# Optimization experiments

Measured on AMD Instinct MI355X. Metric: run time of the kernel, lower is better.

The kernel has to match this reference:

```python
import jax, jax.numpy as jnp
import numpy as np

B = 1024      # batch
DF = 2048     # dim_feat (hard-coded in module)
DIM = 128     # contrastive feature dim
C = 8192      # class_num
P = 8         # pos_size_per_cls
N = 4         # neg_size_per_cls
BN_EPS = 1e-5


def _l2norm(x, axis):
    n = jnp.sqrt(jnp.sum(x * x, axis=axis, keepdims=True))
    return x / jnp.maximum(n, 1e-12)


def setup_inputs() -> dict:
    key = jax.random.key(0)
    ks = jax.random.split(key, 12)
    inp = {
        'mid_feat_q': jax.random.normal(ks[0], (B, DF), jnp.float32),
        'mid_feat_k': jax.random.normal(ks[1], (B, DF), jnp.float32),
        'labels_q': jax.random.randint(ks[2], (B,), 0, C, jnp.int32),
        'labels_k': jax.random.randint(ks[3], (B,), 0, C, jnp.int32),
        'W1': jax.random.normal(ks[4], (DF, DF), jnp.float32) * 0.02,
        'b1': jnp.zeros((DF,), jnp.float32),
        'gamma': jnp.ones((DF,), jnp.float32),
        'beta': jnp.zeros((DF,), jnp.float32),
        'W2': jax.random.normal(ks[5], (DF, DIM), jnp.float32) * 0.02,
        'b2': jnp.zeros((DIM,), jnp.float32),
        'Wlin': jax.random.normal(ks[6], (DF, C), jnp.float32) * 0.02,
        'blin': jnp.zeros((C,), jnp.float32),
        'neg_queue': _l2norm(jax.random.normal(ks[7], (DIM, N * C), jnp.float32), axis=0),
        'pos_queue': _l2norm(jax.random.normal(ks[8], (DIM, P * C), jnp.float32), axis=0),
        'neg_ptr': jnp.zeros((C,), jnp.int32),
        'pos_ptr': jnp.zeros((C,), jnp.int32),
    }
    return inp


def _mlp(x, W1, b1, gamma, beta, W2, b2):
    # Linear -> BatchNorm1d (training: batch stats, biased var) -> ReLU -> Linear
    h = x @ W1 + b1
    mu = jnp.mean(h, axis=0)
    var = jnp.var(h, axis=0)
    h = (h - mu) * jax.lax.rsqrt(var + BN_EPS) * gamma + beta
    h = jax.nn.relu(h)
    return h @ W2 + b2


def reference(mid_feat_q, mid_feat_k, labels_q, labels_k,
              W1, b1, gamma, beta, W2, b2, Wlin, blin,
              neg_queue, pos_queue, neg_ptr, pos_ptr):
    feat_q = _l2norm(_mlp(mid_feat_q, W1, b1, gamma, beta, W2, b2), axis=1)
    feat_k = _l2norm(_mlp(mid_feat_k, W1, b1, gamma, beta, W2, b2), axis=1)

    # per-sample positive block gather: pos_queue[:, l*P:(l+1)*P]
    posq = pos_queue.reshape(DIM, C, P)          # (dim, C, P)
    pg = posq[:, labels_q, :]                    # (dim, B, P)
    pos_list = jnp.einsum('bd,dbp->bp', feat_q, pg)   # (B, P)

    # negatives: full sim then drop each sample's own-class block of N columns
    full_neg = feat_q @ neg_queue                # (B, N*C)
    cols = jnp.arange(N * (C - 1), dtype=jnp.int32)
    idx = cols[None, :] + N * (cols[None, :] >= labels_q[:, None] * N).astype(jnp.int32)
    neg_list = jnp.take_along_axis(full_neg, idx, axis=1)  # (B, N*(C-1))

    sim_batch = feat_q @ feat_k.T                # (B, B)
    labels_batch = (labels_q[:, None] == labels_k[None, :]).astype(jnp.float32)

    sim_con = jnp.concatenate([sim_batch, pos_list, neg_list], axis=1)
    labels_con = jnp.concatenate(
        [labels_batch, jnp.ones_like(pos_list), jnp.zeros_like(neg_list)], axis=1)

    logit_cls_q = mid_feat_q @ Wlin + blin
    logit_cls_k = mid_feat_k @ Wlin + blin

    # sequential dequeue/enqueue over the key batch (world_size=1 all_gather)
    def step(carry, inp):
        nq, nptr, pq, pptr = carry
        kv, c = inp
        npos = nptr[c]
        nq = nq.at[:, c * N + npos].set(kv)
        nptr = nptr.at[c].set((npos + 1) % N)
        ppos = pptr[c]
        pq = pq.at[:, c * P + ppos].set(kv)
        pptr = pptr.at[c].set((ppos + 1) % P)
        return (nq, nptr, pq, pptr), None

    (neg_queue2, neg_ptr2, pos_queue2, pos_ptr2), _ = jax.lax.scan(
        step, (neg_queue, neg_ptr, pos_queue, pos_ptr),
        (jax.lax.stop_gradient(feat_k), labels_k))

    return (sim_con, labels_con, logit_cls_q, logit_cls_k,
            neg_queue2, pos_queue2, neg_ptr2, pos_ptr2)
```

## Files before the change

kernel.cpp:

```cpp
#include <hip/hip_runtime.h>

typedef unsigned short u16;
typedef __bf16 bf16x8 __attribute__((ext_vector_type(8)));
typedef unsigned short ushort8 __attribute__((ext_vector_type(8)));
typedef float f32x4 __attribute__((ext_vector_type(4)));

typedef const __attribute__((address_space(1))) void gv_t;
typedef __attribute__((address_space(3))) void lv_t;

__device__ __forceinline__ u16 f2bf(float f) {
    union { float f; unsigned u; } x; x.f = f;
    unsigned r = x.u + 0x7fffu + ((x.u >> 16) & 1u);
    return (u16)(r >> 16);
}
__device__ __forceinline__ float bf2f(u16 h) {
    union { unsigned u; float f; } x; x.u = ((unsigned)h) << 16; return x.f;
}
__device__ __forceinline__ bf16x8 as_bf(ushort8 u) {
    union { ushort8 u; bf16x8 b; } x; x.u = u; return x.b;
}

__global__ void k_cast2(const float* __restrict__ in0, const float* __restrict__ in1,
                        u16* __restrict__ out0, u16* __restrict__ out1, long nvec) {
    const float* in = blockIdx.y ? in1 : in0;
    u16* out = blockIdx.y ? out1 : out0;
    long i = (long)blockIdx.x * blockDim.x + threadIdx.x;
    long stride = (long)gridDim.x * blockDim.x;
    for (; i < nvec; i += stride) {
        float4 v = ((const float4*)in)[i];
        u16 o[4] = {f2bf(v.x), f2bf(v.y), f2bf(v.z), f2bf(v.w)};
        *(unsigned long long*)(out + i * 4) = *(unsigned long long*)o;
    }
}

__global__ void k_castT(const float* __restrict__ in, u16* __restrict__ out,
                        int R, int C) {
    __shared__ u16 tile[32][33];
    int c0 = blockIdx.x * 32, r0 = blockIdx.y * 32;
    int tx = threadIdx.x, ty = threadIdx.y;
#pragma unroll
    for (int i = 0; i < 4; i++)
        tile[ty + 8 * i][tx] = f2bf(in[(size_t)(r0 + ty + 8 * i) * C + c0 + tx]);
    __syncthreads();
#pragma unroll
    for (int i = 0; i < 4; i++)
        out[(size_t)(c0 + ty + 8 * i) * R + r0 + tx] = tile[tx][ty + 8 * i];
}

template <int EPI>
__global__ __launch_bounds__(256, 2) void gemm_bt(
    const u16* A0, const u16* A1, const u16* __restrict__ Bt,
    const float* __restrict__ bias, u16* H0, u16* H1, float* C0, float* C1,
    int lda, int ldb, long long ldc, int n_tiles, int Kchunk,
    const int* __restrict__ labels) {
    __shared__ u16 Al[128 * 32];
    __shared__ u16 Bl[128 * 32];
    const int bx = blockIdx.x;
    const int by = blockIdx.y % n_tiles;
    const int kc = blockIdx.y / n_tiles;
    const int half = blockIdx.z;
    const u16* A = half ? A1 : A0;
    const int m0 = bx * 128, n0 = by * 128;
    const int t = threadIdx.x;
    const int w = t >> 6, l = t & 63;
    const int wm = (w & 1) * 64, wn = (w >> 1) * 64;
    const int quad = l >> 4, ln = l & 15;
    const int srow = t >> 2;
    const int sk = (t & 3) * 8;

    f32x4 acc[4][4];
#pragma unroll
    for (int i = 0; i < 4; i++)
#pragma unroll
        for (int j = 0; j < 4; j++) acc[i][j] = f32x4{};

    u16* lAw = Al + (w << 4) * 32;
    u16* lBw = Bl + (w << 4) * 32;

    const int k_begin = kc * Kchunk;
    for (int k0 = k_begin; k0 < k_begin + Kchunk; k0 += 32) {
        if (k0 != k_begin) __syncthreads();
#pragma unroll
        for (int i = 0; i < 2; i++) {
            __builtin_amdgcn_global_load_lds(
                (gv_t*)(A + (size_t)(m0 + srow + i * 64) * lda + k0 + sk),
                (lv_t*)(lAw + i * 64 * 32), 16, 0, 0);
            __builtin_amdgcn_global_load_lds(
                (gv_t*)(Bt + (size_t)(n0 + srow + i * 64) * ldb + k0 + sk),
                (lv_t*)(lBw + i * 64 * 32), 16, 0, 0);
        }
        __syncthreads();
        bf16x8 af[4], bb[4];
#pragma unroll
        for (int i = 0; i < 4; i++) {
            af[i] = as_bf(*(const ushort8*)(Al + (wm + i * 16 + ln) * 32 + quad * 8));
            bb[i] = as_bf(*(const ushort8*)(Bl + (wn + i * 16 + ln) * 32 + quad * 8));
        }
#pragma unroll
        for (int i = 0; i < 4; i++)
#pragma unroll
            for (int j = 0; j < 4; j++)
                acc[i][j] = __builtin_amdgcn_mfma_f32_16x16x32_bf16(af[i], bb[j], acc[i][j], 0, 0, 0);
    }

    u16* Hs = half ? H1 : H0;
    float* Cs = half ? C1 : C0;
#pragma unroll
    for (int i = 0; i < 4; i++) {
        int row = m0 + wm + i * 16 + quad * 4;
#pragma unroll
        for (int j = 0; j < 4; j++) {
            int col = n0 + wn + j * 16 + ln;
            float bv = 0.f;
            if (EPI == 0 || EPI == 3) { if (bias) bv = bias[col]; }
#pragma unroll
            for (int r = 0; r < 4; r++) {
                int rr = row + r;
                float v = acc[i][j][r] + bv;
                if (EPI == 0) {
                    Cs[(size_t)rr * ldc + col] = v;
                } else if (EPI == 3) {
                    Hs[(size_t)rr * ldc + col] = f2bf(v);
                } else if (EPI == 2) {
                    Cs[(size_t)kc * (1024 * (size_t)ldc) + (size_t)rr * ldc + col] = v;
                } else {
                    int L4 = labels[rr] * 4;
                    if (col < L4)
                        Cs[(size_t)rr * ldc + 1032 + col] = v;
                    else if (col >= L4 + 4)
                        Cs[(size_t)rr * ldc + 1032 + col - 4] = v;
                }
            }
        }
    }
}

__global__ void k_bn_stats(const u16* __restrict__ Hq, const u16* __restrict__ Hk,
                           float* __restrict__ ps, float* __restrict__ ps2) {
    int half = blockIdx.z;
    const u16* H = half ? Hk : Hq;
    int col = blockIdx.x * 256 + threadIdx.x;
    int r0 = blockIdx.y * 64;
    float s = 0.f, s2 = 0.f;
    for (int r = 0; r < 64; r++) {
        float v = bf2f(H[(size_t)(r0 + r) * 2048 + col]);
        s += v; s2 += v * v;
    }
    size_t o = ((size_t)half * 16 + blockIdx.y) * 2048 + col;
    ps[o] = s; ps2[o] = s2;
}

__global__ void k_bn_final(const float* __restrict__ ps, const float* __restrict__ ps2,
                           const float* __restrict__ gamma, const float* __restrict__ beta,
                           float* __restrict__ scale, float* __restrict__ shift) {
    int idx = blockIdx.x * 256 + threadIdx.x;
    int half = idx >> 11, col = idx & 2047;
    float s = 0.f, s2 = 0.f;
    for (int rb = 0; rb < 16; rb++) {
        size_t o = ((size_t)half * 16 + rb) * 2048 + col;
        s += ps[o]; s2 += ps2[o];
    }
    float mu = s * (1.f / 1024.f);
    float var = s2 * (1.f / 1024.f) - mu * mu;
    float sc = gamma[col] * rsqrtf(var + 1e-5f);
    shift[half * 2048 + col] = beta[col] - mu * sc;
    scale[half * 2048 + col] = sc;
}

__global__ void k_bn_apply(u16* Hq, u16* Hk, const float* __restrict__ scale,
                           const float* __restrict__ shift) {
    int row = blockIdx.x, half = blockIdx.y;
    u16* H = half ? Hk : Hq;
    int col = threadIdx.x * 8;
    ushort8 h = *(ushort8*)(H + (size_t)row * 2048 + col);
    ushort8 o;
#pragma unroll
    for (int k = 0; k < 8; k++) {
        float v = bf2f(h[k]) * scale[half * 2048 + col + k] + shift[half * 2048 + col + k];
        o[k] = f2bf(fmaxf(v, 0.f));
    }
    *(ushort8*)(H + (size_t)row * 2048 + col) = o;
}

__global__ void k_l2norm(const float* __restrict__ Fqp, const float* __restrict__ Fkp,
                         const float* __restrict__ b2, float* fqf, float* fkf,
                         u16* fqh, u16* fkh, const float* __restrict__ pq,
                         const int* __restrict__ lq, float* __restrict__ out0) {
    int row = blockIdx.x, half = blockIdx.y, d = threadIdx.x;
    const float* Fp = half ? Fkp : Fqp;
    float x = b2[d];
#pragma unroll
    for (int kc = 0; kc < 8; kc++)
        x += Fp[(size_t)kc * 131072 + (size_t)row * 128 + d];
    float ss = x * x;
#pragma unroll
    for (int off = 32; off >= 1; off >>= 1) ss += __shfl_down(ss, off);
    __shared__ float p[2];
    if ((threadIdx.x & 63) == 0) p[threadIdx.x >> 6] = ss;
    __syncthreads();
    float n = sqrtf(p[0] + p[1]);
    float v = x / fmaxf(n, 1e-12f);
    (half ? fkf : fqf)[(size_t)row * 128 + d] = v;
    (half ? fkh : fqh)[(size_t)row * 128 + d] = f2bf(v);

    if (half == 0) {
        int base = lq[row] * 8;
        const float* pp = pq + (size_t)d * 65536 + base;
        float4 v0 = *(const float4*)pp;
        float4 v1 = *(const float4*)(pp + 4);
        float a[8] = {v * v0.x, v * v0.y, v * v0.z, v * v0.w,
                      v * v1.x, v * v1.y, v * v1.z, v * v1.w};
#pragma unroll
        for (int off = 32; off >= 1; off >>= 1)
#pragma unroll
            for (int q = 0; q < 8; q++) a[q] += __shfl_down(a[q], off);
        __shared__ float pr[2][8];
        if ((threadIdx.x & 63) == 0) {
#pragma unroll
            for (int q = 0; q < 8; q++) pr[threadIdx.x >> 6][q] = a[q];
        }
        __syncthreads();
        if (threadIdx.x < 8)
            out0[(size_t)row * 33796 + 1024 + threadIdx.x] =
                pr[0][threadIdx.x] + pr[1][threadIdx.x];
    }
}

__global__ void k_labels(const int* __restrict__ lq, const int* __restrict__ lk,
                         float* __restrict__ out1) {
    int b = blockIdx.y;
    int j0 = (blockIdx.x * 256 + threadIdx.x) * 8;
    if (j0 >= 33796) return;
    float* o = out1 + (size_t)b * 33796;
    if (j0 >= 1032 && j0 + 8 <= 33796) {
        float4 z = {0.f, 0.f, 0.f, 0.f};
        *(float4*)(o + j0) = z;
        *(float4*)(o + j0 + 4) = z;
    } else {
        int Lq = lq[b];
        for (int k = 0; k < 8 && j0 + k < 33796; k++) {
            int j = j0 + k;
            o[j] = (j < 1024) ? ((Lq == lk[j]) ? 1.f : 0.f) : (j < 1032 ? 1.f : 0.f);
        }
    }
}

__global__ void k_copy2(const float* __restrict__ s1, float* __restrict__ d1, long n1,
                        const float* __restrict__ s2, float* __restrict__ d2, long n2) {
    long i = (long)blockIdx.x * blockDim.x + threadIdx.x;
    long stride = (long)gridDim.x * blockDim.x;
    long tot = n1 + n2;
    for (; i < tot; i += stride) {
        if (i < n1) ((float4*)d1)[i] = ((const float4*)s1)[i];
        else ((float4*)d2)[i - n1] = ((const float4*)s2)[i - n1];
    }
}

__global__ void k_rank(const int* __restrict__ lk, const int* __restrict__ nptr,
                       const int* __restrict__ pptr, int* __restrict__ counts,
                       int* __restrict__ colN, int* __restrict__ colP) {
    __shared__ int lab[1024];
    int tid = threadIdx.x;
    for (int i = tid; i < 1024; i += 128) lab[i] = lk[i];
    __syncthreads();
    int b = blockIdx.x * 128 + tid;
    int c = lab[b];
    int rank = 0, count = 0;
    for (int i = 0; i < 1024; i++) {
        int m = (lab[i] == c);
        count += m;
        rank += (i < b) ? m : 0;
    }
    if (rank == count - 1) counts[c] = count;
    colN[b] = (rank >= count - 4) ? c * 4 + (nptr[c] + rank) % 4 : -1;
    colP[b] = (rank >= count - 8) ? c * 8 + (pptr[c] + rank) % 8 : -1;
}

__global__ void k_scatter(const float* __restrict__ fkf, const int* __restrict__ colN,
                          const int* __restrict__ colP, float* outN, float* outP) {
    int b = blockIdx.x, d = threadIdx.x;
    float v = fkf[(size_t)b * 128 + d];
    int cn = colN[b];
    if (cn >= 0) outN[(size_t)d * 32768 + cn] = v;
    int cp = colP[b];
    if (cp >= 0) outP[(size_t)d * 65536 + cp] = v;
}

__global__ void k_ptrs(const int* __restrict__ nptr, const int* __restrict__ pptr,
                       const int* __restrict__ counts, float* outN, float* outP) {
    int c = blockIdx.x * 256 + threadIdx.x;
    int cnt = counts[c];
    outN[c] = (float)((nptr[c] + cnt) & 3);
    outP[c] = (float)((pptr[c] + cnt) & 7);
}

extern "C" void kernel_launch(void* const* d_in, const int* in_sizes, int n_in,
                              void* d_out, int out_size, void* d_ws, size_t ws_size,
                              hipStream_t stream) {
    const float* midq = (const float*)d_in[0];
    const float* midk = (const float*)d_in[1];
    const int* lq     = (const int*)d_in[2];
    const int* lk     = (const int*)d_in[3];
    const float* W1   = (const float*)d_in[4];
    const float* b1   = (const float*)d_in[5];
    const float* gamma= (const float*)d_in[6];
    const float* beta = (const float*)d_in[7];
    const float* W2   = (const float*)d_in[8];
    const float* b2   = (const float*)d_in[9];
    const float* Wlin = (const float*)d_in[10];
    const float* blin = (const float*)d_in[11];
    const float* nq   = (const float*)d_in[12];
    const float* pq   = (const float*)d_in[13];
    const int* nptr   = (const int*)d_in[14];
    const int* pptr   = (const int*)d_in[15];
    (void)in_sizes; (void)n_in; (void)out_size; (void)ws_size;

    float* out = (float*)d_out;
    const size_t O0 = 0;
    const size_t O1 = 34607104;
    const size_t O2 = 69214208;
    const size_t O3 = 77602816;
    const size_t O4 = 85991424;
    const size_t O5 = 90185728;
    const size_t O6 = 98574336;
    const size_t O7 = 98582528;

    char* ws = (char*)d_ws;
    size_t off = 0;
    auto alloc = [&](size_t bytes) -> char* {
        char* p = ws + off;
        off = (off + bytes + 255) & ~(size_t)255;
        return p;
    };
    u16* W1t   = (u16*)alloc((size_t)2048 * 2048 * 2);
    u16* WlinT = (u16*)alloc((size_t)8192 * 2048 * 2);
    u16* W2t   = (u16*)alloc((size_t)128 * 2048 * 2);
    u16* nqT   = (u16*)alloc((size_t)32768 * 128 * 2);
    u16* midqh = (u16*)alloc((size_t)1024 * 2048 * 2);
    u16* midkh = (u16*)alloc((size_t)1024 * 2048 * 2);
    u16* Hq    = (u16*)alloc((size_t)1024 * 2048 * 2);
    u16* Hk    = (u16*)alloc((size_t)1024 * 2048 * 2);
    float* Fq  = (float*)alloc((size_t)8 * 1024 * 128 * 4);
    float* Fk  = (float*)alloc((size_t)8 * 1024 * 128 * 4);
    float* fqf = (float*)alloc((size_t)1024 * 128 * 4);
    float* fkf = (float*)alloc((size_t)1024 * 128 * 4);
    u16* fqh   = (u16*)alloc((size_t)1024 * 128 * 2);
    u16* fkh   = (u16*)alloc((size_t)1024 * 128 * 2);
    float* ps  = (float*)alloc((size_t)2 * 16 * 2048 * 4);
    float* ps2 = (float*)alloc((size_t)2 * 16 * 2048 * 4);
    float* scaleA = (float*)alloc((size_t)2 * 2048 * 4);
    float* shiftA = (float*)alloc((size_t)2 * 2048 * 4);
    int* counts = (int*)alloc(8192 * 4);
    int* colN   = (int*)alloc(1024 * 4);
    int* colP   = (int*)alloc(1024 * 4);

    k_cast2<<<dim3(1024, 2), 256, 0, stream>>>(midq, midk, midqh, midkh,
                                               (long)1024 * 2048 / 4);
    dim3 tb(32, 8);
    k_castT<<<dim3(64, 64), tb, 0, stream>>>(W1, W1t, 2048, 2048);
    k_castT<<<dim3(256, 64), tb, 0, stream>>>(Wlin, WlinT, 2048, 8192);
    k_castT<<<dim3(4, 64), tb, 0, stream>>>(W2, W2t, 2048, 128);
    k_castT<<<dim3(1024, 4), tb, 0, stream>>>(nq, nqT, 128, 32768);

    gemm_bt<3><<<dim3(8, 16, 2), 256, 0, stream>>>(midqh, midkh, W1t, b1, Hq, Hk,
        nullptr, nullptr, 2048, 2048, 2048, 16, 2048, nullptr);

    k_bn_stats<<<dim3(8, 16, 2), 256, 0, stream>>>(Hq, Hk, ps, ps2);
    k_bn_final<<<16, 256, 0, stream>>>(ps, ps2, gamma, beta, scaleA, shiftA);
    k_bn_apply<<<dim3(1024, 2), 256, 0, stream>>>(Hq, Hk, scaleA, shiftA);

    hipMemsetAsync(counts, 0, 8192 * 4, stream);

    gemm_bt<2><<<dim3(8, 8, 2), 256, 0, stream>>>(Hq, Hk, W2t, nullptr, nullptr,
        nullptr, Fq, Fk, 2048, 2048, 128, 1, 256, nullptr);

    k_l2norm<<<dim3(1024, 2), 128, 0, stream>>>(Fq, Fk, b2, fqf, fkf, fqh, fkh,
                                                pq, lq, out + O0);

    gemm_bt<0><<<dim3(8, 8, 1), 256, 0, stream>>>(fqh, fqh, fkh, nullptr,
        nullptr, nullptr, out + O0, out + O0, 128, 128, 33796, 8, 128, nullptr);

    gemm_bt<1><<<dim3(8, 256, 1), 256, 0, stream>>>(fqh, fqh, nqT, nullptr,
        nullptr, nullptr, out + O0, out + O0, 128, 128, 33796, 256, 128, lq);

    k_labels<<<dim3(17, 1024), 256, 0, stream>>>(lq, lk, out + O1);

    gemm_bt<0><<<dim3(8, 64, 2), 256, 0, stream>>>(midqh, midkh, WlinT, blin,
        nullptr, nullptr, out + O2, out + O3, 2048, 2048, 8192, 64, 2048, nullptr);

    k_copy2<<<2048, 256, 0, stream>>>(nq, out + O4, 4194304 / 4,
                                      pq, out + O5, 8388608 / 4);

    k_rank<<<8, 128, 0, stream>>>(lk, nptr, pptr, counts, colN, colP);
    k_scatter<<<1024, 128, 0, stream>>>(fkf, colN, colP, out + O4, out + O5);
    k_ptrs<<<32, 256, 0, stream>>>(nptr, pptr, counts, out + O6, out + O7);
}
```

Baseline: 775.9 us.

## Double GEMM K-tile to 64 with XOR-swizzled LDS; fuse BN-stats and scatter kernels

The bf16 MFMA GEMM now stages 64-wide K slices per iteration instead of 32. Rows are written into LDS with an XOR swizzle of 8-element chunks, and fragments are read back with the matching swizzle. This halves the barrier and load-issue overhead per unit of K and is meant to cut LDS bank conflicts on fragment reads. BatchNorm statistics are computed in one kernel, with each thread summing all 1024 rows of a column, which drops the partial-sum buffers and a launch but runs only 16 blocks. The queue scatter and pointer-update kernels are merged into one launch.

```diff
diff --git a/kernel.cpp b/kernel.cpp
--- a/kernel.cpp
+++ b/kernel.cpp
@@ -53,8 +53,8 @@
     const float* __restrict__ bias, u16* H0, u16* H1, float* C0, float* C1,
     int lda, int ldb, long long ldc, int n_tiles, int Kchunk,
     const int* __restrict__ labels) {
-    __shared__ u16 Al[128 * 32];
-    __shared__ u16 Bl[128 * 32];
+    __shared__ u16 Al[128 * 64];
+    __shared__ u16 Bl[128 * 64];
     const int bx = blockIdx.x;
     const int by = blockIdx.y % n_tiles;
     const int kc = blockIdx.y / n_tiles;
@@ -65,8 +65,8 @@
     const int w = t >> 6, l = t & 63;
     const int wm = (w & 1) * 64, wn = (w >> 1) * 64;
     const int quad = l >> 4, ln = l & 15;
-    const int srow = t >> 2;
-    const int sk = (t & 3) * 8;
+    const int srow = t >> 3;
+    const int spos = t & 7;
 
     f32x4 acc[4][4];
 #pragma unroll
@@ -74,33 +74,38 @@
 #pragma unroll
         for (int j = 0; j < 4; j++) acc[i][j] = f32x4{};
 
-    u16* lAw = Al + (w << 4) * 32;
-    u16* lBw = Bl + (w << 4) * 32;
+    const int swz = ln & 7;
 
     const int k_begin = kc * Kchunk;
-    for (int k0 = k_begin; k0 < k_begin + Kchunk; k0 += 32) {
+    for (int k0 = k_begin; k0 < k_begin + Kchunk; k0 += 64) {
         if (k0 != k_begin) __syncthreads();
 #pragma unroll
-        for (int i = 0; i < 2; i++) {
+        for (int i = 0; i < 4; i++) {
+            int r = i * 32 + srow;
+            int c = (spos ^ (r & 7)) * 8;
             __builtin_amdgcn_global_load_lds(
-                (gv_t*)(A + (size_t)(m0 + srow + i * 64) * lda + k0 + sk),
-                (lv_t*)(lAw + i * 64 * 32), 16, 0, 0);
+                (gv_t*)(A + (size_t)(m0 + r) * lda + k0 + c),
+                (lv_t*)(Al + i * 2048 + t * 8), 16, 0, 0);
             __builtin_amdgcn_global_load_lds(
-                (gv_t*)(Bt + (size_t)(n0 + srow + i * 64) * ldb + k0 + sk),
-                (lv_t*)(lBw + i * 64 * 32), 16, 0, 0);
+                (gv_t*)(Bt + (size_t)(n0 + r) * ldb + k0 + c),
+                (lv_t*)(Bl + i * 2048 + t * 8), 16, 0, 0);
         }
         __syncthreads();
-        bf16x8 af[4], bb[4];
-#pragma unroll
-        for (int i = 0; i < 4; i++) {
-            af[i] = as_bf(*(const ushort8*)(Al + (wm + i * 16 + ln) * 32 + quad * 8));
-            bb[i] = as_bf(*(const ushort8*)(Bl + (wn + i * 16 + ln) * 32 + quad * 8));
-        }
-#pragma unroll
-        for (int i = 0; i < 4; i++)
-#pragma unroll
-            for (int j = 0; j < 4; j++)
-                acc[i][j] = __builtin_amdgcn_mfma_f32_16x16x32_bf16(af[i], bb[j], acc[i][j], 0, 0, 0);
+#pragma unroll
+        for (int ks = 0; ks < 2; ks++) {
+            bf16x8 af[4], bb[4];
+#pragma unroll
+            for (int i = 0; i < 4; i++) {
+                int cc = ((ks * 4 + quad) ^ swz) * 8;
+                af[i] = as_bf(*(const ushort8*)(Al + (wm + i * 16 + ln) * 64 + cc));
+                bb[i] = as_bf(*(const ushort8*)(Bl + (wn + i * 16 + ln) * 64 + cc));
+            }
+#pragma unroll
+            for (int i = 0; i < 4; i++)
+#pragma unroll
+                for (int j = 0; j < 4; j++)
+                    acc[i][j] = __builtin_amdgcn_mfma_f32_16x16x32_bf16(af[i], bb[j], acc[i][j], 0, 0, 0);
+        }
     }
 
     u16* Hs = half ? H1 : H0;
@@ -135,30 +140,17 @@
     }
 }
 
-__global__ void k_bn_stats(const u16* __restrict__ Hq, const u16* __restrict__ Hk,
-                           float* __restrict__ ps, float* __restrict__ ps2) {
-    int half = blockIdx.z;
+__global__ void k_bn(const u16* __restrict__ Hq, const u16* __restrict__ Hk,
+                     const float* __restrict__ gamma, const float* __restrict__ beta,
+                     float* __restrict__ scale, float* __restrict__ shift) {
+    int half = blockIdx.y;
     const u16* H = half ? Hk : Hq;
     int col = blockIdx.x * 256 + threadIdx.x;
-    int r0 = blockIdx.y * 64;
     float s = 0.f, s2 = 0.f;
-    for (int r = 0; r < 64; r++) {
-        float v = bf2f(H[(size_t)(r0 + r) * 2048 + col]);
+#pragma unroll 8
+    for (int r = 0; r < 1024; r++) {
+        float v = bf2f(H[(size_t)r * 2048 + col]);
         s += v; s2 += v * v;
-    }
-    size_t o = ((size_t)half * 16 + blockIdx.y) * 2048 + col;
-    ps[o] = s; ps2[o] = s2;
-}
-
-__global__ void k_bn_final(const float* __restrict__ ps, const float* __restrict__ ps2,
-                           const float* __restrict__ gamma, const float* __restrict__ beta,
-                           float* __restrict__ scale, float* __restrict__ shift) {
-    int idx = blockIdx.x * 256 + threadIdx.x;
-    int half = idx >> 11, col = idx & 2047;
-    float s = 0.f, s2 = 0.f;
-    for (int rb = 0; rb < 16; rb++) {
-        size_t o = ((size_t)half * 16 + rb) * 2048 + col;
-        s += ps[o]; s2 += ps2[o];
     }
     float mu = s * (1.f / 1024.f);
     float var = s2 * (1.f / 1024.f) - mu * mu;
@@ -276,22 +268,26 @@
     colP[b] = (rank >= count - 8) ? c * 8 + (pptr[c] + rank) % 8 : -1;
 }
 
-__global__ void k_scatter(const float* __restrict__ fkf, const int* __restrict__ colN,
-                          const int* __restrict__ colP, float* outN, float* outP) {
-    int b = blockIdx.x, d = threadIdx.x;
-    float v = fkf[(size_t)b * 128 + d];
-    int cn = colN[b];
-    if (cn >= 0) outN[(size_t)d * 32768 + cn] = v;
-    int cp = colP[b];
-    if (cp >= 0) outP[(size_t)d * 65536 + cp] = v;
-}
-
-__global__ void k_ptrs(const int* __restrict__ nptr, const int* __restrict__ pptr,
-                       const int* __restrict__ counts, float* outN, float* outP) {
-    int c = blockIdx.x * 256 + threadIdx.x;
-    int cnt = counts[c];
-    outN[c] = (float)((nptr[c] + cnt) & 3);
-    outP[c] = (float)((pptr[c] + cnt) & 7);
+__global__ void k_scatter_ptrs(const float* __restrict__ fkf,
+                               const int* __restrict__ colN, const int* __restrict__ colP,
+                               const int* __restrict__ nptr, const int* __restrict__ pptr,
+                               const int* __restrict__ counts,
+                               float* outN, float* outP, float* outNp, float* outPp) {
+    int bid = blockIdx.x;
+    if (bid < 512) {
+        int b = bid * 2 + (threadIdx.x >> 7);
+        int d = threadIdx.x & 127;
+        float v = fkf[(size_t)b * 128 + d];
+        int cn = colN[b];
+        if (cn >= 0) outN[(size_t)d * 32768 + cn] = v;
+        int cp = colP[b];
+        if (cp >= 0) outP[(size_t)d * 65536 + cp] = v;
+    } else {
+        int c = (bid - 512) * 256 + threadIdx.x;
+        int cnt = counts[c];
+        outNp[c] = (float)((nptr[c] + cnt) & 3);
+        outPp[c] = (float)((pptr[c] + cnt) & 7);
+    }
 }
 
 extern "C" void kernel_launch(void* const* d_in, const int* in_sizes, int n_in,
@@ -346,8 +342,6 @@
     float* fkf = (float*)alloc((size_t)1024 * 128 * 4);
     u16* fqh   = (u16*)alloc((size_t)1024 * 128 * 2);
     u16* fkh   = (u16*)alloc((size_t)1024 * 128 * 2);
-    float* ps  = (float*)alloc((size_t)2 * 16 * 2048 * 4);
-    float* ps2 = (float*)alloc((size_t)2 * 16 * 2048 * 4);
     float* scaleA = (float*)alloc((size_t)2 * 2048 * 4);
     float* shiftA = (float*)alloc((size_t)2 * 2048 * 4);
     int* counts = (int*)alloc(8192 * 4);
@@ -365,8 +359,7 @@
     gemm_bt<3><<<dim3(8, 16, 2), 256, 0, stream>>>(midqh, midkh, W1t, b1, Hq, Hk,
         nullptr, nullptr, 2048, 2048, 2048, 16, 2048, nullptr);
 
-    k_bn_stats<<<dim3(8, 16, 2), 256, 0, stream>>>(Hq, Hk, ps, ps2);
-    k_bn_final<<<16, 256, 0, stream>>>(ps, ps2, gamma, beta, scaleA, shiftA);
+    k_bn<<<dim3(8, 2), 256, 0, stream>>>(Hq, Hk, gamma, beta, scaleA, shiftA);
     k_bn_apply<<<dim3(1024, 2), 256, 0, stream>>>(Hq, Hk, scaleA, shiftA);
 
     hipMemsetAsync(counts, 0, 8192 * 4, stream);
@@ -392,6 +385,6 @@
                                       pq, out + O5, 8388608 / 4);
 
     k_rank<<<8, 128, 0, stream>>>(lk, nptr, pptr, counts, colN, colP);
-    k_scatter<<<1024, 128, 0, stream>>>(fkf, colN, colP, out + O4, out + O5);
-    k_ptrs<<<32, 256, 0, stream>>>(nptr, pptr, counts, out + O6, out + O7);
-}
+    k_scatter_ptrs<<<544, 256, 0, stream>>>(fkf, colN, colP, nptr, pptr, counts,
+                                            out + O4, out + O5, out + O6, out + O7);
+}
```

Result: slower. 806.3 us (+3.9%).

## Merge same-input GEMM launches and small tail kernels into combined launches

Applied to the files above, without the earlier changes.

The W1 projection GEMM and the classifier (Wlin) GEMM share the same mid-feature A operand, so they now run as one 80-tile-wide launch with a per-tile epilogue. That launch also remaps block IDs so each XCD works on a contiguous group of N tiles. The sim_batch GEMM and the negative-queue GEMM are likewise fused into one launch that picks its B matrix per tile, and the scatter and pointer-update kernels become a single kernel. The aim is fewer launches, better wave fill and better L2 reuse of A. It relies on WlinT sitting right after W1t in the workspace so the combined B indexing stays valid.

```diff
diff --git a/kernel.cpp b/kernel.cpp
--- a/kernel.cpp
+++ b/kernel.cpp
@@ -50,17 +50,33 @@
 template <int EPI>
 __global__ __launch_bounds__(256, 2) void gemm_bt(
     const u16* A0, const u16* A1, const u16* __restrict__ Bt,
-    const float* __restrict__ bias, u16* H0, u16* H1, float* C0, float* C1,
+    const u16* __restrict__ Bt2, const float* __restrict__ bias,
+    const float* __restrict__ bias2, u16* H0, u16* H1, float* C0, float* C1,
     int lda, int ldb, long long ldc, int n_tiles, int Kchunk,
     const int* __restrict__ labels) {
     __shared__ u16 Al[128 * 32];
     __shared__ u16 Bl[128 * 32];
-    const int bx = blockIdx.x;
-    const int by = blockIdx.y % n_tiles;
-    const int kc = blockIdx.y / n_tiles;
-    const int half = blockIdx.z;
+
+    int bx, by, kc, half;
+    if (EPI == 4) {
+        int pid = blockIdx.x + blockIdx.y * 8 + blockIdx.z * 640;
+        int xcd = pid & 7, idx = pid >> 3;
+        by = xcd * 10 + idx % 10;
+        int rem = idx / 10;
+        bx = rem & 7; half = rem >> 3; kc = 0;
+    } else if (EPI == 5) {
+        bx = blockIdx.x; by = blockIdx.y; kc = 0; half = 0;
+    } else {
+        bx = blockIdx.x; by = blockIdx.y % n_tiles; kc = blockIdx.y / n_tiles;
+        half = blockIdx.z;
+    }
     const u16* A = half ? A1 : A0;
-    const int m0 = bx * 128, n0 = by * 128;
+
+    const u16* B = Bt;
+    int bn0 = by * 128;
+    if (EPI == 5 && by >= 8) { B = Bt2; bn0 = (by - 8) * 128; }
+
+    const int m0 = bx * 128;
     const int t = threadIdx.x;
     const int w = t >> 6, l = t & 63;
     const int wm = (w & 1) * 64, wn = (w >> 1) * 64;
@@ -86,7 +102,7 @@
                 (gv_t*)(A + (size_t)(m0 + srow + i * 64) * lda + k0 + sk),
                 (lv_t*)(lAw + i * 64 * 32), 16, 0, 0);
             __builtin_amdgcn_global_load_lds(
-                (gv_t*)(Bt + (size_t)(n0 + srow + i * 64) * ldb + k0 + sk),
+                (gv_t*)(B + (size_t)(bn0 + srow + i * 64) * ldb + k0 + sk),
                 (lv_t*)(lBw + i * 64 * 32), 16, 0, 0);
         }
         __syncthreads();
@@ -103,32 +119,42 @@
                 acc[i][j] = __builtin_amdgcn_mfma_f32_16x16x32_bf16(af[i], bb[j], acc[i][j], 0, 0, 0);
     }
 
-    u16* Hs = half ? H1 : H0;
-    float* Cs = half ? C1 : C0;
 #pragma unroll
     for (int i = 0; i < 4; i++) {
         int row = m0 + wm + i * 16 + quad * 4;
 #pragma unroll
         for (int j = 0; j < 4; j++) {
-            int col = n0 + wn + j * 16 + ln;
-            float bv = 0.f;
-            if (EPI == 0 || EPI == 3) { if (bias) bv = bias[col]; }
+            int cl = wn + j * 16 + ln;
 #pragma unroll
             for (int r = 0; r < 4; r++) {
                 int rr = row + r;
-                float v = acc[i][j][r] + bv;
-                if (EPI == 0) {
-                    Cs[(size_t)rr * ldc + col] = v;
-                } else if (EPI == 3) {
-                    Hs[(size_t)rr * ldc + col] = f2bf(v);
-                } else if (EPI == 2) {
+                float v = acc[i][j][r];
+                if (EPI == 2) {
+                    int col = by * 128 + cl;
+                    float* Cs = half ? C1 : C0;
                     Cs[(size_t)kc * (1024 * (size_t)ldc) + (size_t)rr * ldc + col] = v;
-                } else {
-                    int L4 = labels[rr] * 4;
-                    if (col < L4)
-                        Cs[(size_t)rr * ldc + 1032 + col] = v;
-                    else if (col >= L4 + 4)
-                        Cs[(size_t)rr * ldc + 1032 + col - 4] = v;
+                } else if (EPI == 4) {
+                    if (by < 16) {
+                        int col = by * 128 + cl;
+                        u16* Hs = half ? H1 : H0;
+                        Hs[(size_t)rr * 2048 + col] = f2bf(v + bias[col]);
+                    } else {
+                        int col = (by - 16) * 128 + cl;
+                        float* Cs = half ? C1 : C0;
+                        Cs[(size_t)rr * 8192 + col] = v + bias2[col];
+                    }
+                } else if (EPI == 5) {
+                    if (by < 8) {
+                        int col = by * 128 + cl;
+                        C0[(size_t)rr * 33796 + col] = v;
+                    } else {
+                        int col = (by - 8) * 128 + cl;
+                        int L4 = labels[rr] * 4;
+                        if (col < L4)
+                            C0[(size_t)rr * 33796 + 1032 + col] = v;
+                        else if (col >= L4 + 4)
+                            C0[(size_t)rr * 33796 + 1032 + col - 4] = v;
+                    }
                 }
             }
         }
@@ -276,22 +302,26 @@
     colP[b] = (rank >= count - 8) ? c * 8 + (pptr[c] + rank) % 8 : -1;
 }
 
-__global__ void k_scatter(const float* __restrict__ fkf, const int* __restrict__ colN,
-                          const int* __restrict__ colP, float* outN, float* outP) {
-    int b = blockIdx.x, d = threadIdx.x;
-    float v = fkf[(size_t)b * 128 + d];
-    int cn = colN[b];
-    if (cn >= 0) outN[(size_t)d * 32768 + cn] = v;
-    int cp = colP[b];
-    if (cp >= 0) outP[(size_t)d * 65536 + cp] = v;
-}
-
-__global__ void k_ptrs(const int* __restrict__ nptr, const int* __restrict__ pptr,
-                       const int* __restrict__ counts, float* outN, float* outP) {
-    int c = blockIdx.x * 256 + threadIdx.x;
-    int cnt = counts[c];
-    outN[c] = (float)((nptr[c] + cnt) & 3);
-    outP[c] = (float)((pptr[c] + cnt) & 7);
+__global__ void k_scatter_ptrs(const float* __restrict__ fkf,
+                               const int* __restrict__ colN, const int* __restrict__ colP,
+                               const int* __restrict__ nptr, const int* __restrict__ pptr,
+                               const int* __restrict__ counts,
+                               float* outN, float* outP, float* outNp, float* outPp) {
+    int bid = blockIdx.x;
+    if (bid < 512) {
+        int b = bid * 2 + (threadIdx.x >> 7);
+        int d = threadIdx.x & 127;
+        float v = fkf[(size_t)b * 128 + d];
+        int cn = colN[b];
+        if (cn >= 0) outN[(size_t)d * 32768 + cn] = v;
+        int cp = colP[b];
+        if (cp >= 0) outP[(size_t)d * 65536 + cp] = v;
+    } else {
+        int c = (bid - 512) * 256 + threadIdx.x;
+        int cnt = counts[c];
+        outNp[c] = (float)((nptr[c] + cnt) & 3);
+        outPp[c] = (float)((pptr[c] + cnt) & 7);
+    }
 }
 
 extern "C" void kernel_launch(void* const* d_in, const int* in_sizes, int n_in,
@@ -362,8 +392,8 @@
     k_castT<<<dim3(4, 64), tb, 0, stream>>>(W2, W2t, 2048, 128);
     k_castT<<<dim3(1024, 4), tb, 0, stream>>>(nq, nqT, 128, 32768);
 
-    gemm_bt<3><<<dim3(8, 16, 2), 256, 0, stream>>>(midqh, midkh, W1t, b1, Hq, Hk,
-        nullptr, nullptr, 2048, 2048, 2048, 16, 2048, nullptr);
+    gemm_bt<4><<<dim3(8, 80, 2), 256, 0, stream>>>(midqh, midkh, W1t, nullptr,
+        b1, blin, Hq, Hk, out + O2, out + O3, 2048, 2048, 0, 80, 2048, nullptr);
 
     k_bn_stats<<<dim3(8, 16, 2), 256, 0, stream>>>(Hq, Hk, ps, ps2);
     k_bn_final<<<16, 256, 0, stream>>>(ps, ps2, gamma, beta, scaleA, shiftA);
@@ -372,26 +402,21 @@
     hipMemsetAsync(counts, 0, 8192 * 4, stream);
 
     gemm_bt<2><<<dim3(8, 8, 2), 256, 0, stream>>>(Hq, Hk, W2t, nullptr, nullptr,
-        nullptr, Fq, Fk, 2048, 2048, 128, 1, 256, nullptr);
+        nullptr, nullptr, nullptr, Fq, Fk, 2048, 2048, 128, 1, 256, nullptr);
 
     k_l2norm<<<dim3(1024, 2), 128, 0, stream>>>(Fq, Fk, b2, fqf, fkf, fqh, fkh,
                                                 pq, lq, out + O0);
 
-    gemm_bt<0><<<dim3(8, 8, 1), 256, 0, stream>>>(fqh, fqh, fkh, nullptr,
-        nullptr, nullptr, out + O0, out + O0, 128, 128, 33796, 8, 128, nullptr);
-
-    gemm_bt<1><<<dim3(8, 256, 1), 256, 0, stream>>>(fqh, fqh, nqT, nullptr,
-        nullptr, nullptr, out + O0, out + O0, 128, 128, 33796, 256, 128, lq);
+    gemm_bt<5><<<dim3(8, 264, 1), 256, 0, stream>>>(fqh, fqh, fkh, nqT,
+        nullptr, nullptr, nullptr, nullptr, out + O0, out + O0,
+        128, 128, 33796, 264, 128, lq);
 
     k_labels<<<dim3(17, 1024), 256, 0, stream>>>(lq, lk, out + O1);
-
-    gemm_bt<0><<<dim3(8, 64, 2), 256, 0, stream>>>(midqh, midkh, WlinT, blin,
-        nullptr, nullptr, out + O2, out + O3, 2048, 2048, 8192, 64, 2048, nullptr);
 
     k_copy2<<<2048, 256, 0, stream>>>(nq, out + O4, 4194304 / 4,
                                       pq, out + O5, 8388608 / 4);
 
     k_rank<<<8, 128, 0, stream>>>(lk, nptr, pptr, counts, colN, colP);
-    k_scatter<<<1024, 128, 0, stream>>>(fkf, colN, colP, out + O4, out + O5);
-    k_ptrs<<<32, 256, 0, stream>>>(nptr, pptr, counts, out + O6, out + O7);
-}
+    k_scatter_ptrs<<<544, 256, 0, stream>>>(fkf, colN, colP, nptr, pptr, counts,
+                                            out + O4, out + O5, out + O6, out + O7);
+}
```

New measurement: 766.1 us. About the same (-1.3%).
